# Kernel tuning notes

Hardware: AMD Instinct MI355X
Metric: run time of the kernel (lower is better)

Reference implementation:

```python
import jax, jax.numpy as jnp
import numpy as np

N_HEADS = 16


def setup_inputs() -> dict:
    key = jax.random.key(0)
    k1, k2 = jax.random.split(key)
    bs, width, length = 8, 3 * N_HEADS * 64, 1024  # C=64 per head
    qkv = jax.random.normal(k1, (bs, width, length), dtype=jnp.float32)
    mask = jax.random.uniform(k2, (bs, length), dtype=jnp.float32)
    return {"qkv": qkv, "mask": mask}


def reference(qkv, mask):
    bs, width, length = qkv.shape
    ch = width // (3 * N_HEADS)
    q, k, v = jnp.split(qkv, 3, axis=1)
    # view(bs*H, ch, T): head index is inner (b*H + h ordering)
    q = q.reshape(bs * N_HEADS, ch, length)
    k = k.reshape(bs * N_HEADS, ch, length)
    v = v.reshape(bs * N_HEADS, ch, length)
    scale = 1.0 / jnp.sqrt(jnp.sqrt(jnp.asarray(ch, dtype=qkv.dtype)))
    # [bs*H, T, T] score matrix
    weight = jnp.einsum('bct,bcs->bts', q * scale, k * scale)
    # torch mask.repeat(n_heads, 1) tiles the batch dim -> jnp.tile
    m = jnp.tile(mask, (N_HEADS, 1))[:, None, :]  # [bs*H, 1, T]
    weight = weight * m
    weight = jax.nn.softmax(weight.astype(jnp.float32), axis=-1).astype(weight.dtype)
    a = jnp.einsum('bts,bcs->bct', weight, v)  # [bs*H, ch, T]
    return a.reshape(bs, N_HEADS * ch, length)
```

## Files before the change

kernel.cpp:

```cpp
#include <hip/hip_runtime.h>
#include <stdint.h>
#include <math.h>

typedef float  f32x4  __attribute__((ext_vector_type(4)));
typedef __bf16 bf16x8 __attribute__((ext_vector_type(8)));
typedef __bf16 bf16x4 __attribute__((ext_vector_type(4)));

#define MFMA16(a, b, c) __builtin_amdgcn_mfma_f32_16x16x32_bf16((a), (b), (c), 0, 0, 0)
#define EXP2(x) __builtin_amdgcn_exp2f(x)

static constexpr int kT = 1024;

static constexpr int kTileEl = 4096;
static constexpr size_t kTensorEl    = (size_t)128 * 16 * kTileEl;
static constexpr size_t kTensorBytes = kTensorEl * 2;

static constexpr int kLS = 72;

__device__ inline void async16(const void* g, void* l) {
  __builtin_amdgcn_global_load_lds(
      (const __attribute__((address_space(1))) void*)g,
      (__attribute__((address_space(3))) void*)l, 16, 0, 0);
}

__global__ __launch_bounds__(256, 8)
void prepass(const float* __restrict__ qkv, const float* __restrict__ mask,
             __bf16* __restrict__ kh, __bf16* __restrict__ vh)
{
  __shared__ float ts[64 * 65];
  const int tid = threadIdx.x;
  const int bid = blockIdx.x, bh = bid >> 4, tile = bid & 15;
  const int b = bh >> 4, h = bh & 15, t0 = tile * 64;
  const float* __restrict__ kb = qkv + (size_t)(b * 3072 + 1024 + h * 64) * kT;
  const float* __restrict__ vb = qkv + (size_t)(b * 3072 + 2048 + h * 64) * kT;
  const float* __restrict__ mrow = mask + (size_t)(h & 7) * kT;
  const size_t tbase = ((size_t)bh * 16 + tile) * kTileEl;

  const int t4   = (tid & 15) * 4;
  const int crow = tid >> 4;
  const f32x4 m4 = *(const f32x4*)&mrow[t0 + t4];
  #pragma unroll
  for (int i = 0; i < 4; ++i) {
    const int c = i * 16 + crow;
    f32x4 k4 = *(const f32x4*)&kb[(size_t)c * kT + t0 + t4];
    k4 *= m4;
    *(f32x4*)&ts[c * 65 + t4] = k4;
  }
  __syncthreads();

  #pragma unroll
  for (int i = 0; i < 2; ++i) {
    const int p = i * 256 + tid;
    const int chunk = p >> 6, pl = p & 63;
    const int vc  = (chunk >> 1) * 16 + (pl & 15);
    const int vs0 = (chunk & 1) * 32 + (pl >> 4) * 8;
    const f32x4 va  = *(const f32x4*)&vb[(size_t)vc * kT + t0 + vs0];
    const f32x4 vbq = *(const f32x4*)&vb[(size_t)vc * kT + t0 + vs0 + 4];
    const int ks  = (chunk >> 1) * 16 + (pl & 15);
    const int kc0 = (chunk & 1) * 32 + (pl >> 4) * 8;
    bf16x8 k8, v8;
    #pragma unroll
    for (int j = 0; j < 8; ++j) k8[j] = (__bf16)ts[(kc0 + j) * 65 + ks];
    #pragma unroll
    for (int j = 0; j < 4; ++j) { v8[j] = (__bf16)va[j]; v8[4 + j] = (__bf16)vbq[j]; }
    *(bf16x8*)&kh[tbase + (size_t)p * 8] = k8;
    *(bf16x8*)&vh[tbase + (size_t)p * 8] = v8;
  }
}

__global__ __launch_bounds__(256, 4)
void attn_main(const float* __restrict__ qkv,
               const __bf16* __restrict__ kh, const __bf16* __restrict__ vh,
               float* __restrict__ out)
{
  __shared__ __align__(16) char smem[32768];

  const int tid  = threadIdx.x;
  const int lane = tid & 63;
  const int wave = tid >> 6;
  const int quad = lane >> 4;
  const int l15  = lane & 15;

  const int bid = blockIdx.x;
  const int bh  = bid & 127;
  const int tp  = bid >> 7;
  const int b   = bh >> 4;
  const int h   = bh & 15;
  const int t0  = tp * 128;
  const size_t hbase = (size_t)bh * 16;

  bf16x8 qh[2][2], ql[2][2];
  {
    float* ts = (float*)smem;
    const float* __restrict__ qb = qkv + (size_t)(b * 3072 + h * 64) * kT;
    const int t4   = (tid & 15) * 4;
    const int crow = tid >> 4;
    const int trow = wave * 16 + l15;
    #pragma unroll
    for (int half = 0; half < 2; ++half) {
      const int tq0 = t0 + half * 64;
      #pragma unroll
      for (int i = 0; i < 4; ++i) {
        const int c = i * 16 + crow;
        f32x4 q4 = *(const f32x4*)&qb[(size_t)c * kT + tq0 + t4];
        q4 *= 0.18033688f;
        *(f32x4*)&ts[c * 65 + t4] = q4;
      }
      __syncthreads();
      #pragma unroll
      for (int kc = 0; kc < 2; ++kc) {
        bf16x8 hf, lf;
        #pragma unroll
        for (int j = 0; j < 8; ++j) {
          float q = ts[(kc * 32 + quad * 8 + j) * 65 + trow];
          __bf16 hi = (__bf16)q;
          hf[j] = hi;
          lf[j] = (__bf16)(q - (float)hi);
        }
        qh[half][kc] = hf;
        ql[half][kc] = lf;
      }
      __syncthreads();
    }
  }

  {
    const char* g = (const char*)(kh + hbase * kTileEl) + (size_t)lane * 16;
    for (int i = wave; i < 8; i += 4) async16(g + i * 1024, smem + i * 1024);
  }

  f32x4 O0[4], O1[4];
  #pragma unroll
  for (int cc = 0; cc < 4; ++cc) {
    O0[cc] = (f32x4){0.f, 0.f, 0.f, 0.f};
    O1[cc] = (f32x4){0.f, 0.f, 0.f, 0.f};
  }
  float ls0 = 0.f, ls1 = 0.f;

  char* sP0 = smem + 16384 + wave * 4096;
  char* sP1 = sP0 + 2048;
  const int pwr = (l15 << 4) + ((quad & 1) << 3) + ((quad >> 1) << 8);

  for (int st = 0; st < 16; ++st) {
    __syncthreads();

    const __bf16* __restrict__ vt = vh + (hbase + st) * kTileEl;

    bf16x8 vf0[4], vf1[4];
    #pragma unroll
    for (int cc = 0; cc < 4; ++cc)
      vf0[cc] = *(const bf16x8*)&vt[(size_t)(cc * 2) * 512 + lane * 8];

    if (st < 15) {
      const char* g = (const char*)(kh + (hbase + st + 1) * kTileEl) + (size_t)lane * 16;
      char* l = smem + ((st + 1) & 1) * 8192;
      for (int i = wave; i < 8; i += 4) async16(g + i * 1024, l + i * 1024);
    }

    const __bf16* __restrict__ sKc = (const __bf16*)(smem + (st & 1) * 8192);

    __builtin_amdgcn_s_setprio(1);

    #pragma unroll
    for (int sc = 0; sc < 4; ++sc) {
      bf16x8 k0 = *(const bf16x8*)&sKc[(size_t)(sc * 2) * 512 + lane * 8];
      bf16x8 k1 = *(const bf16x8*)&sKc[(size_t)(sc * 2 + 1) * 512 + lane * 8];
      f32x4 a0 = (f32x4){0.f, 0.f, 0.f, 0.f};
      f32x4 a1 = (f32x4){0.f, 0.f, 0.f, 0.f};
      a0 = MFMA16(k0, ql[0][0], a0);
      a1 = MFMA16(k0, ql[1][0], a1);
      a0 = MFMA16(k0, qh[0][0], a0);
      a1 = MFMA16(k0, qh[1][0], a1);
      a0 = MFMA16(k1, ql[0][1], a0);
      a1 = MFMA16(k1, ql[1][1], a1);
      a0 = MFMA16(k1, qh[0][1], a0);
      a1 = MFMA16(k1, qh[1][1], a1);
      bf16x4 p0, p1;
      #pragma unroll
      for (int r = 0; r < 4; ++r) {
        float e0 = EXP2(a0[r]);
        float e1 = EXP2(a1[r]);
        ls0 += e0;
        ls1 += e1;
        p0[r] = (__bf16)e0;
        p1[r] = (__bf16)e1;
      }
      const int po = ((sc >> 1) << 10) + ((sc & 1) << 9) + pwr;
      *(bf16x4*)(sP0 + po) = p0;
      *(bf16x4*)(sP1 + po) = p1;
    }

    #pragma unroll
    for (int cc = 0; cc < 4; ++cc)
      vf1[cc] = *(const bf16x8*)&vt[(size_t)(cc * 2 + 1) * 512 + lane * 8];

    bf16x8 pb00 = *(const bf16x8*)(sP0 + lane * 16);
    bf16x8 pb01 = *(const bf16x8*)(sP0 + 1024 + lane * 16);
    bf16x8 pb10 = *(const bf16x8*)(sP1 + lane * 16);
    bf16x8 pb11 = *(const bf16x8*)(sP1 + 1024 + lane * 16);

    #pragma unroll
    for (int cc = 0; cc < 4; ++cc) {
      O0[cc] = MFMA16(vf0[cc], pb00, O0[cc]);
      O1[cc] = MFMA16(vf0[cc], pb10, O1[cc]);
      O0[cc] = MFMA16(vf1[cc], pb01, O0[cc]);
      O1[cc] = MFMA16(vf1[cc], pb11, O1[cc]);
    }

    __builtin_amdgcn_s_setprio(0);
  }

  ls0 += __shfl_xor(ls0, 16);
  ls0 += __shfl_xor(ls0, 32);
  ls1 += __shfl_xor(ls1, 16);
  ls1 += __shfl_xor(ls1, 32);
  const float inv0 = 1.0f / ls0;
  const float inv1 = 1.0f / ls1;

  const int tcol = t0 + wave * 16 + l15;
  float* __restrict__ obase = out + (size_t)b * (1024 * 1024) + (size_t)(h * 64) * kT;
  #pragma unroll
  for (int cc = 0; cc < 4; ++cc) {
    #pragma unroll
    for (int r = 0; r < 4; ++r) {
      const int c = cc * 16 + quad * 4 + r;
      obase[(size_t)c * kT + tcol]      = O0[cc][r] * inv0;
      obase[(size_t)c * kT + tcol + 64] = O1[cc][r] * inv1;
    }
  }
}

__global__ __launch_bounds__(256, 2)
void attn_fused(const float* __restrict__ qkv, const float* __restrict__ mask,
                float* __restrict__ out)
{
  __shared__ __align__(16) __bf16 Ahi[64 * kLS];
  __shared__ __align__(16) __bf16 Alo[64 * kLS];
  __shared__ __align__(16) __bf16 Vhi[64 * kLS];
  __shared__ __align__(16) __bf16 Vlo[64 * kLS];
  __shared__ __align__(16) __bf16 Phi[64 * kLS];
  __shared__ __align__(16) __bf16 Plo[64 * kLS];
  __shared__ __align__(16) float  ms[64];

  const int tid  = threadIdx.x;
  const int lane = tid & 63;
  const int wave = tid >> 6;
  const int quad = lane >> 4;
  const int l15  = lane & 15;

  const int bid = blockIdx.x;
  const int bh  = bid >> 4;
  const int tb  = bid & 15;
  const int b   = bh >> 4;
  const int h   = bh & 15;
  const int t0  = tb * 64;

  const float* __restrict__ qbase = qkv + (size_t)(b * 3072 + h * 64) * kT;
  const float* __restrict__ kbase = qkv + (size_t)(b * 3072 + 1024 + h * 64) * kT;
  const float* __restrict__ vbase = qkv + (size_t)(b * 3072 + 2048 + h * 64) * kT;
  const float* __restrict__ mrow  = mask + (size_t)(h & 7) * kT;

  const int sl = tid & 63;
  const int cg = tid >> 6;

  #pragma unroll
  for (int i = 0; i < 16; ++i) {
    const int c = cg * 16 + i;
    float v  = qbase[(size_t)c * kT + t0 + sl] * 0.125f;
    __bf16 hi = (__bf16)v;
    Ahi[sl * kLS + c] = hi;
    Alo[sl * kLS + c] = (__bf16)(v - (float)hi);
  }
  __syncthreads();

  bf16x8 qh[2], ql[2];
  {
    const int row = (wave * 16 + l15) * kLS;
    #pragma unroll
    for (int kc = 0; kc < 2; ++kc) {
      qh[kc] = *(const bf16x8*)&Ahi[row + kc * 32 + quad * 8];
      ql[kc] = *(const bf16x8*)&Alo[row + kc * 32 + quad * 8];
    }
  }
  __syncthreads();

  f32x4 O[4];
  #pragma unroll
  for (int cc = 0; cc < 4; ++cc) O[cc] = (f32x4){0.f, 0.f, 0.f, 0.f};
  float m_run = -__builtin_inff();
  float l_run = 0.f;

  for (int s0 = 0; s0 < kT; s0 += 64) {
    #pragma unroll
    for (int i = 0; i < 16; ++i) {
      const int c = cg * 16 + i;
      float kv   = kbase[(size_t)c * kT + s0 + sl];
      __bf16 khi = (__bf16)kv;
      Ahi[sl * kLS + c] = khi;
      Alo[sl * kLS + c] = (__bf16)(kv - (float)khi);
      float vv   = vbase[(size_t)c * kT + s0 + sl];
      __bf16 vhi = (__bf16)vv;
      Vhi[c * kLS + sl] = vhi;
      Vlo[c * kLS + sl] = (__bf16)(vv - (float)vhi);
    }
    if (tid < 64) ms[tid] = mrow[s0 + tid];
    __syncthreads();

    f32x4 S[4];
    #pragma unroll
    for (int sc = 0; sc < 4; ++sc) {
      f32x4 acc = (f32x4){0.f, 0.f, 0.f, 0.f};
      #pragma unroll
      for (int kc = 0; kc < 2; ++kc) {
        const int off = (sc * 16 + l15) * kLS + kc * 32 + quad * 8;
        bf16x8 kh8 = *(const bf16x8*)&Ahi[off];
        bf16x8 kl8 = *(const bf16x8*)&Alo[off];
        acc = MFMA16(kh8, ql[kc], acc);
        acc = MFMA16(kl8, qh[kc], acc);
        acc = MFMA16(kh8, qh[kc], acc);
      }
      S[sc] = acc;
    }

    float x[16];
    float tmax = -__builtin_inff();
    #pragma unroll
    for (int sc = 0; sc < 4; ++sc) {
      f32x4 mv = *(const f32x4*)&ms[sc * 16 + quad * 4];
      #pragma unroll
      for (int r = 0; r < 4; ++r) {
        float xv = S[sc][r] * mv[r];
        x[sc * 4 + r] = xv;
        tmax = fmaxf(tmax, xv);
      }
    }
    tmax = fmaxf(tmax, __shfl_xor(tmax, 16));
    tmax = fmaxf(tmax, __shfl_xor(tmax, 32));
    const float mnew  = fmaxf(m_run, tmax);
    const float alpha = __expf(m_run - mnew);
    float tsum = 0.f;
    #pragma unroll
    for (int i = 0; i < 16; ++i) {
      float p = __expf(x[i] - mnew);
      x[i] = p;
      tsum += p;
    }
    tsum += __shfl_xor(tsum, 16);
    tsum += __shfl_xor(tsum, 32);
    l_run = l_run * alpha + tsum;
    m_run = mnew;
    #pragma unroll
    for (int cc = 0; cc < 4; ++cc) O[cc] = O[cc] * alpha;

    const int prow = (wave * 16 + l15) * kLS;
    #pragma unroll
    for (int sc = 0; sc < 4; ++sc) {
      bf16x4 ph, pl;
      #pragma unroll
      for (int r = 0; r < 4; ++r) {
        float p   = x[sc * 4 + r];
        __bf16 hi = (__bf16)p;
        ph[r] = hi;
        pl[r] = (__bf16)(p - (float)hi);
      }
      *(bf16x4*)&Phi[prow + sc * 16 + quad * 4] = ph;
      *(bf16x4*)&Plo[prow + sc * 16 + quad * 4] = pl;
    }
    __syncthreads();

    bf16x8 pbh[2], pbl[2];
    #pragma unroll
    for (int kc = 0; kc < 2; ++kc) {
      pbh[kc] = *(const bf16x8*)&Phi[prow + kc * 32 + quad * 8];
      pbl[kc] = *(const bf16x8*)&Plo[prow + kc * 32 + quad * 8];
    }
    #pragma unroll
    for (int cc = 0; cc < 4; ++cc) {
      #pragma unroll
      for (int kc = 0; kc < 2; ++kc) {
        const int off = (cc * 16 + l15) * kLS + kc * 32 + quad * 8;
        bf16x8 v8 = *(const bf16x8*)&Vhi[off];
        bf16x8 w8 = *(const bf16x8*)&Vlo[off];
        O[cc] = MFMA16(v8, pbl[kc], O[cc]);
        O[cc] = MFMA16(w8, pbh[kc], O[cc]);
        O[cc] = MFMA16(v8, pbh[kc], O[cc]);
      }
    }
    __syncthreads();
  }

  const float inv  = 1.0f / l_run;
  const int   tcol = t0 + wave * 16 + l15;
  float* __restrict__ obase = out + (size_t)b * (1024 * 1024) + (size_t)(h * 64) * kT;
  #pragma unroll
  for (int cc = 0; cc < 4; ++cc) {
    #pragma unroll
    for (int r = 0; r < 4; ++r) {
      const int c = cc * 16 + quad * 4 + r;
      obase[(size_t)c * kT + tcol] = O[cc][r] * inv;
    }
  }
}

extern "C" void kernel_launch(void* const* d_in, const int* in_sizes, int n_in,
                              void* d_out, int out_size, void* d_ws, size_t ws_size,
                              hipStream_t stream)
{
  const float* qkv  = (const float*)d_in[0];
  const float* mask = (const float*)d_in[1];
  float* out = (float*)d_out;
  (void)in_sizes; (void)n_in; (void)out_size;

  if (ws_size >= 2 * kTensorBytes) {
    char* w = (char*)d_ws;
    __bf16* kh = (__bf16*)(w + 0 * kTensorBytes);
    __bf16* vh = (__bf16*)(w + 1 * kTensorBytes);
    prepass<<<dim3(2048), dim3(256), 0, stream>>>(qkv, mask, kh, vh);
    attn_main<<<dim3(1024), dim3(256), 0, stream>>>(qkv, kh, vh, out);
  } else {
    attn_fused<<<dim3(2048), dim3(256), 0, stream>>>(qkv, mask, out);
  }
}
```

Baseline: 212.0 us.

## Process two K/V tiles per barrier with larger double-buffered K prefetch

The main loop now handles two 64-key tiles per iteration, prefetching 16 KB of K per stage into a double buffer so there are half as many __syncthreads and async-load issue points. The row-sum accumulation becomes a 4-wide vector of partial sums instead of a serial scalar chain, which shortens the dependency on the exponent results. The s_setprio hints are dropped. Shared memory grows to 48 KB and launch bounds fall from 4 to 3 blocks per SIMD, which may lower occupancy and latency hiding.

```diff
diff --git a/kernel.cpp b/kernel.cpp
--- a/kernel.cpp
+++ b/kernel.cpp
@@ -68,12 +68,12 @@
   }
 }
 
-__global__ __launch_bounds__(256, 4)
+__global__ __launch_bounds__(256, 3)
 void attn_main(const float* __restrict__ qkv,
                const __bf16* __restrict__ kh, const __bf16* __restrict__ vh,
                float* __restrict__ out)
 {
-  __shared__ __align__(16) char smem[32768];
+  __shared__ __align__(16) char smem[49152];
 
   const int tid  = threadIdx.x;
   const int lane = tid & 63;
@@ -126,7 +126,7 @@
 
   {
     const char* g = (const char*)(kh + hbase * kTileEl) + (size_t)lane * 16;
-    for (int i = wave; i < 8; i += 4) async16(g + i * 1024, smem + i * 1024);
+    for (int i = wave; i < 16; i += 4) async16(g + i * 1024, smem + i * 1024);
   }
 
   f32x4 O0[4], O1[4];
@@ -135,81 +135,86 @@
     O0[cc] = (f32x4){0.f, 0.f, 0.f, 0.f};
     O1[cc] = (f32x4){0.f, 0.f, 0.f, 0.f};
   }
-  float ls0 = 0.f, ls1 = 0.f;
-
-  char* sP0 = smem + 16384 + wave * 4096;
+  f32x4 la0 = (f32x4){0.f, 0.f, 0.f, 0.f};
+  f32x4 la1 = (f32x4){0.f, 0.f, 0.f, 0.f};
+
+  char* sP0 = smem + 32768 + wave * 4096;
   char* sP1 = sP0 + 2048;
   const int pwr = (l15 << 4) + ((quad & 1) << 3) + ((quad >> 1) << 8);
 
-  for (int st = 0; st < 16; ++st) {
+  for (int p = 0; p < 8; ++p) {
     __syncthreads();
 
-    const __bf16* __restrict__ vt = vh + (hbase + st) * kTileEl;
-
-    bf16x8 vf0[4], vf1[4];
-    #pragma unroll
-    for (int cc = 0; cc < 4; ++cc)
-      vf0[cc] = *(const bf16x8*)&vt[(size_t)(cc * 2) * 512 + lane * 8];
-
-    if (st < 15) {
-      const char* g = (const char*)(kh + (hbase + st + 1) * kTileEl) + (size_t)lane * 16;
-      char* l = smem + ((st + 1) & 1) * 8192;
-      for (int i = wave; i < 8; i += 4) async16(g + i * 1024, l + i * 1024);
-    }
-
-    const __bf16* __restrict__ sKc = (const __bf16*)(smem + (st & 1) * 8192);
-
-    __builtin_amdgcn_s_setprio(1);
-
-    #pragma unroll
-    for (int sc = 0; sc < 4; ++sc) {
-      bf16x8 k0 = *(const bf16x8*)&sKc[(size_t)(sc * 2) * 512 + lane * 8];
-      bf16x8 k1 = *(const bf16x8*)&sKc[(size_t)(sc * 2 + 1) * 512 + lane * 8];
-      f32x4 a0 = (f32x4){0.f, 0.f, 0.f, 0.f};
-      f32x4 a1 = (f32x4){0.f, 0.f, 0.f, 0.f};
-      a0 = MFMA16(k0, ql[0][0], a0);
-      a1 = MFMA16(k0, ql[1][0], a1);
-      a0 = MFMA16(k0, qh[0][0], a0);
-      a1 = MFMA16(k0, qh[1][0], a1);
-      a0 = MFMA16(k1, ql[0][1], a0);
-      a1 = MFMA16(k1, ql[1][1], a1);
-      a0 = MFMA16(k1, qh[0][1], a0);
-      a1 = MFMA16(k1, qh[1][1], a1);
-      bf16x4 p0, p1;
-      #pragma unroll
-      for (int r = 0; r < 4; ++r) {
-        float e0 = EXP2(a0[r]);
-        float e1 = EXP2(a1[r]);
-        ls0 += e0;
-        ls1 += e1;
-        p0[r] = (__bf16)e0;
-        p1[r] = (__bf16)e1;
-      }
-      const int po = ((sc >> 1) << 10) + ((sc & 1) << 9) + pwr;
-      *(bf16x4*)(sP0 + po) = p0;
-      *(bf16x4*)(sP1 + po) = p1;
-    }
-
-    #pragma unroll
-    for (int cc = 0; cc < 4; ++cc)
-      vf1[cc] = *(const bf16x8*)&vt[(size_t)(cc * 2 + 1) * 512 + lane * 8];
-
-    bf16x8 pb00 = *(const bf16x8*)(sP0 + lane * 16);
-    bf16x8 pb01 = *(const bf16x8*)(sP0 + 1024 + lane * 16);
-    bf16x8 pb10 = *(const bf16x8*)(sP1 + lane * 16);
-    bf16x8 pb11 = *(const bf16x8*)(sP1 + 1024 + lane * 16);
-
-    #pragma unroll
-    for (int cc = 0; cc < 4; ++cc) {
-      O0[cc] = MFMA16(vf0[cc], pb00, O0[cc]);
-      O1[cc] = MFMA16(vf0[cc], pb10, O1[cc]);
-      O0[cc] = MFMA16(vf1[cc], pb01, O0[cc]);
-      O1[cc] = MFMA16(vf1[cc], pb11, O1[cc]);
-    }
-
-    __builtin_amdgcn_s_setprio(0);
-  }
-
+    if (p < 7) {
+      const char* g = (const char*)(kh + (hbase + 2 * (p + 1)) * kTileEl) + (size_t)lane * 16;
+      char* l = smem + ((p + 1) & 1) * 16384;
+      for (int i = wave; i < 16; i += 4) async16(g + i * 1024, l + i * 1024);
+    }
+
+    #pragma unroll
+    for (int u = 0; u < 2; ++u) {
+      const __bf16* __restrict__ vt  = vh + (hbase + 2 * p + u) * kTileEl;
+      const __bf16* __restrict__ sKt = (const __bf16*)(smem + (p & 1) * 16384 + u * 8192);
+
+      bf16x8 vf0[4], vf1[4];
+      #pragma unroll
+      for (int cc = 0; cc < 4; ++cc)
+        vf0[cc] = *(const bf16x8*)&vt[(size_t)(cc * 2) * 512 + lane * 8];
+
+      #pragma unroll
+      for (int sc = 0; sc < 4; ++sc) {
+        bf16x8 k0 = *(const bf16x8*)&sKt[(size_t)(sc * 2) * 512 + lane * 8];
+        bf16x8 k1 = *(const bf16x8*)&sKt[(size_t)(sc * 2 + 1) * 512 + lane * 8];
+        f32x4 a0 = (f32x4){0.f, 0.f, 0.f, 0.f};
+        f32x4 a1 = (f32x4){0.f, 0.f, 0.f, 0.f};
+        a0 = MFMA16(k0, ql[0][0], a0);
+        a1 = MFMA16(k0, ql[1][0], a1);
+        a0 = MFMA16(k0, qh[0][0], a0);
+        a1 = MFMA16(k0, qh[1][0], a1);
+        a0 = MFMA16(k1, ql[0][1], a0);
+        a1 = MFMA16(k1, ql[1][1], a1);
+        a0 = MFMA16(k1, qh[0][1], a0);
+        a1 = MFMA16(k1, qh[1][1], a1);
+        f32x4 e0, e1;
+        #pragma unroll
+        for (int r = 0; r < 4; ++r) {
+          e0[r] = EXP2(a0[r]);
+          e1[r] = EXP2(a1[r]);
+        }
+        la0 += e0;
+        la1 += e1;
+        bf16x4 p0, p1;
+        #pragma unroll
+        for (int r = 0; r < 4; ++r) {
+          p0[r] = (__bf16)e0[r];
+          p1[r] = (__bf16)e1[r];
+        }
+        const int po = ((sc >> 1) << 10) + ((sc & 1) << 9) + pwr;
+        *(bf16x4*)(sP0 + po) = p0;
+        *(bf16x4*)(sP1 + po) = p1;
+      }
+
+      #pragma unroll
+      for (int cc = 0; cc < 4; ++cc)
+        vf1[cc] = *(const bf16x8*)&vt[(size_t)(cc * 2 + 1) * 512 + lane * 8];
+
+      bf16x8 pb00 = *(const bf16x8*)(sP0 + lane * 16);
+      bf16x8 pb01 = *(const bf16x8*)(sP0 + 1024 + lane * 16);
+      bf16x8 pb10 = *(const bf16x8*)(sP1 + lane * 16);
+      bf16x8 pb11 = *(const bf16x8*)(sP1 + 1024 + lane * 16);
+
+      #pragma unroll
+      for (int cc = 0; cc < 4; ++cc) {
+        O0[cc] = MFMA16(vf0[cc], pb00, O0[cc]);
+        O1[cc] = MFMA16(vf0[cc], pb10, O1[cc]);
+        O0[cc] = MFMA16(vf1[cc], pb01, O0[cc]);
+        O1[cc] = MFMA16(vf1[cc], pb11, O1[cc]);
+      }
+    }
+  }
+
+  float ls0 = la0[0] + la0[1] + la0[2] + la0[3];
+  float ls1 = la1[0] + la1[1] + la1[2] + la1[3];
   ls0 += __shfl_xor(ls0, 16);
   ls0 += __shfl_xor(ls0, 32);
   ls1 += __shfl_xor(ls1, 16);
```

Result: faster. 204.9 us (-3.3%).
